# Kernel optimization log

Measured on AMD Instinct MI355X. Metric: run time of the kernel, lower is better.

## Reference

```python
import jax, jax.numpy as jnp
import numpy as np

N = 100000
E = 1600000
IN_F = 16
OUT_F = 16
HEADS = 6
ALPHA_COEFF = 0.2
NEG_SLOPE = 0.2


def setup_inputs() -> dict:
    key = jax.random.key(0)
    k1, k2, k3, k4, k5, k6 = jax.random.split(key, 6)
    data = jax.random.uniform(k1, (N, IN_F), dtype=jnp.float32)
    edge_index = jax.random.randint(k2, (2, E), 0, N, dtype=jnp.int64)
    # GATConv params (glorot-ish scale)
    W = jax.random.normal(k3, (IN_F, HEADS * OUT_F), dtype=jnp.float32) * (1.0 / np.sqrt(IN_F))
    att_src = jax.random.normal(k4, (1, HEADS, OUT_F), dtype=jnp.float32) * (1.0 / np.sqrt(OUT_F))
    att_dst = jax.random.normal(k5, (1, HEADS, OUT_F), dtype=jnp.float32) * (1.0 / np.sqrt(OUT_F))
    bias = jnp.zeros((OUT_F,), dtype=jnp.float32)
    return {"data": data, "edge_index": edge_index, "W": W,
            "att_src": att_src, "att_dst": att_dst, "bias": bias}


def _gat_deformer(data, edge_index, W, att_src, att_dst, bias):
    n = data.shape[0]
    # add self loops (PyG GATConv default add_self_loops=True)
    loop = jnp.arange(n, dtype=edge_index.dtype)
    src = jnp.concatenate([edge_index[0], loop])  # [E']
    dst = jnp.concatenate([edge_index[1], loop])  # [E']

    x = (data @ W).reshape(n, HEADS, OUT_F)          # [N,H,C]
    a_src = jnp.sum(x * att_src, axis=-1)            # [N,H]
    a_dst = jnp.sum(x * att_dst, axis=-1)            # [N,H]

    e = a_src[src] + a_dst[dst]                      # [E',H]
    e = jnp.where(e > 0, e, NEG_SLOPE * e)           # leaky_relu(0.2)
    # segment softmax over destination nodes (PyG softmax, +1e-16 denom)
    seg_max = jax.ops.segment_max(e, dst, num_segments=n)
    e = jnp.exp(e - seg_max[dst])
    seg_sum = jax.ops.segment_sum(e, dst, num_segments=n)
    alpha = e / (seg_sum[dst] + 1e-16)               # [E',H]

    # first pass: weighted scatter-add of transformed features
    out = jax.ops.segment_sum(x[src] * alpha[:, :, None], dst, num_segments=n)  # [N,H,C]
    feat = out.mean(axis=1) + bias                   # concat=False -> head mean, + bias

    # second propagate: reuse (scaled) attention on raw coordinates
    coord = data[:, :2]                              # [N,2]
    alpha2 = alpha * ALPHA_COEFF                     # [E',H]
    msg = coord[src][:, None, :] * alpha2[:, :, None]  # [E',H,2]
    out_coord = jax.ops.segment_sum(msg, dst, num_segments=n).mean(axis=1)  # [N,2]

    # fix boundary nodes (masks computed from input coords)
    up = data[:, 0] == 1.0
    down = data[:, 0] == 0.0
    left = data[:, 1] == 0.0
    right = data[:, 1] == 1.0
    c0 = jnp.where(up, 1.0, jnp.where(down, 0.0, out_coord[:, 0]))
    c1 = jnp.where(right, 1.0, jnp.where(left, 0.0, out_coord[:, 1]))
    out_coord = jnp.stack([c0, c1], axis=1)

    feat = jax.nn.selu(feat)
    return out_coord, feat


def reference(data, edge_index, W, att_src, att_dst, bias):
    return _gat_deformer(data, edge_index, W, att_src, att_dst, bias)
```

## Files before the change

kernel.cpp:

```cpp
#include <hip/hip_runtime.h>
#include <hip/hip_fp16.h>
#include <math.h>

#define N_NODES 100000
#define N_EDGES 1600000
#define E_TOT (N_EDGES + N_NODES)
#define IN_FEAT 16
#define OUT_FEAT 16
#define HEADS 6
#define HF 96

#define NB 4096
#define NBA 4000
#define NPB 25
#define CAP 576
#define MAXDEG 64
#define NBLK_PART 256
#define NT_BLOCKS ((N_NODES * HEADS + 255) / 256)

static __device__ __forceinline__ unsigned int pk2h(float a, float b) {
    return (unsigned int)__half_as_ushort(__float2half_rn(a))
         | ((unsigned int)__half_as_ushort(__float2half_rn(b)) << 16);
}

__global__ void prep(const int* __restrict__ esrc,
                     const int* __restrict__ edst,
                     int* __restrict__ gcursor,
                     unsigned int* __restrict__ spack,
                     const float* __restrict__ data,
                     const float* __restrict__ W,
                     const float* __restrict__ att_src,
                     const float* __restrict__ att_dst,
                     float* __restrict__ a_srcF,
                     float* __restrict__ a_dstF,
                     unsigned short* __restrict__ data_f16) {
    __shared__ int shmem[2 * NB];

    if (blockIdx.x < NBLK_PART) {
        int* hist = shmem;
        int* base = shmem + NB;
        const int chunk = (E_TOT + NBLK_PART - 1) / NBLK_PART;
        const int e0 = blockIdx.x * chunk;
        const int e1 = min(e0 + chunk, E_TOT);

        for (int j = threadIdx.x; j < NB; j += blockDim.x) hist[j] = 0;
        __syncthreads();
        for (int e = e0 + threadIdx.x; e < e1; e += blockDim.x) {
            int d = (e < N_EDGES) ? edst[e] : (e - N_EDGES);
            atomicAdd(&hist[d / NPB], 1);
        }
        __syncthreads();
        for (int j = threadIdx.x; j < NB; j += blockDim.x) {
            int c = hist[j];
            base[j] = c ? atomicAdd(&gcursor[j], c) : 0;
        }
        __syncthreads();
        for (int j = threadIdx.x; j < NB; j += blockDim.x) hist[j] = 0;
        __syncthreads();
        for (int e = e0 + threadIdx.x; e < e1; e += blockDim.x) {
            int s, d;
            if (e < N_EDGES) { s = esrc[e]; d = edst[e]; }
            else             { s = d = e - N_EDGES; }
            int b = d / NPB;
            int r = atomicAdd(&hist[b], 1);
            int pos = b * CAP + base[b] + r;
            if (pos < (b + 1) * CAP)
                spack[pos] = (unsigned int)s | ((unsigned int)(d - b * NPB) << 17);
        }
    } else {
        float* sW  = (float*)shmem;
        float* sAs = sW + IN_FEAT * HF;
        float* sAd = sAs + HF;
        for (int i = threadIdx.x; i < IN_FEAT * HF; i += blockDim.x) sW[i] = W[i];
        for (int i = threadIdx.x; i < HF; i += blockDim.x) { sAs[i] = att_src[i]; sAd[i] = att_dst[i]; }
        __syncthreads();

        int gid = (blockIdx.x - NBLK_PART) * blockDim.x + threadIdx.x;
        int n = gid / HEADS;
        int h = gid % HEADS;
        if (n >= N_NODES) return;

        float dv[IN_FEAT];
        const float4* dp = (const float4*)(data + (size_t)n * IN_FEAT);
#pragma unroll
        for (int q = 0; q < 4; q++) {
            float4 v = dp[q];
            dv[q*4+0] = v.x; dv[q*4+1] = v.y; dv[q*4+2] = v.z; dv[q*4+3] = v.w;
        }

        if (h < 4) {
            uint2 pkd;
            pkd.x = pk2h(dv[h*4+0], dv[h*4+1]);
            pkd.y = pk2h(dv[h*4+2], dv[h*4+3]);
            *(uint2*)(data_f16 + (size_t)n * IN_FEAT + h * 4) = pkd;
        }

        float outv[OUT_FEAT];
#pragma unroll
        for (int fo = 0; fo < OUT_FEAT; fo++) outv[fo] = 0.f;
#pragma unroll
        for (int k = 0; k < IN_FEAT; k++) {
            float dk = dv[k];
            const float* wrow = &sW[k * HF + h * OUT_FEAT];
#pragma unroll
            for (int fo = 0; fo < OUT_FEAT; fo++) outv[fo] = fmaf(dk, wrow[fo], outv[fo]);
        }

        float as = 0.f, ad = 0.f;
#pragma unroll
        for (int fo = 0; fo < OUT_FEAT; fo++) {
            as = fmaf(outv[fo], sAs[h * OUT_FEAT + fo], as);
            ad = fmaf(outv[fo], sAd[h * OUT_FEAT + fo], ad);
        }
        a_srcF[n * 8 + h] = as;
        a_dstF[n * 8 + h] = ad;
        if (h == 0) {
            a_srcF[n * 8 + 6] = 0.f; a_srcF[n * 8 + 7] = 0.f;
            a_dstF[n * 8 + 6] = 0.f; a_dstF[n * 8 + 7] = 0.f;
        }
    }
}

__global__ __launch_bounds__(256, 4)
void bucket_accumulate(const int* __restrict__ gcursor,
                       const unsigned int* __restrict__ spack,
                       const float* __restrict__ data,
                       const unsigned short* __restrict__ data_f16,
                       const float* __restrict__ a_srcF,
                       const float* __restrict__ a_dstF,
                       const float* __restrict__ W,
                       const float* __restrict__ bias,
                       float* __restrict__ out) {
    const int b = blockIdx.x;
    const int n0 = b * NPB;
    __shared__ unsigned int olist[NPB * MAXDEG];
    __shared__ float wsn_l[NPB * 100];
    __shared__ int cnt[NPB];
    __shared__ int nidx;

    const int tid  = threadIdx.x;
    const int lane = tid & 63;
    const int slot = lane >> 4;
    const int f    = lane & 15;
    const int sbase = lane & 48;

    int ecnt = gcursor[b];
    if (ecnt > CAP) ecnt = CAP;

    for (int j = tid; j < NPB; j += 256) cnt[j] = 0;
    if (tid == 0) nidx = 0;
    __syncthreads();

    for (int i = tid; i < ecnt; i += 256) {
        unsigned int p = spack[b * CAP + i];
        int dl = (int)(p >> 17);
        int r = atomicAdd(&cnt[dl], 1);
        if (r < MAXDEG)
            olist[dl * MAXDEG + r] = p & 0x1FFFFu;
    }
    __syncthreads();

    for (;;) {
        int my;
        if (lane == 0) my = atomicAdd(&nidx, 1);
        my = __builtin_amdgcn_readfirstlane(my);
        if (my >= NPB) break;

        int T = cnt[my];
        if (T > MAXDEG) T = MAXDEG;
        const unsigned int* ol = olist + my * MAXDEG;

        float adh = 0.f;
        if (f < HEADS) adh = a_dstF[(n0 + my) * 8 + f];

        float ws[HEADS], dn[HEADS];
#pragma unroll
        for (int h = 0; h < HEADS; h++) { ws[h] = 0.f; dn[h] = 0.f; }

        for (int t = slot; t < T; t += 4) {
            int s = (int)ol[t];
            float dv = __half2float(__ushort_as_half(data_f16[(size_t)s * IN_FEAT + f]));
            float exv = 0.f;
            if (f < HEADS) {
                float e = a_srcF[s * 8 + f] + adh;
                e = fmaxf(e, 0.2f * e);
                exv = __expf(e);
            }
            float e0 = __shfl(exv, sbase + 0);
            float e1 = __shfl(exv, sbase + 1);
            float e2 = __shfl(exv, sbase + 2);
            float e3 = __shfl(exv, sbase + 3);
            float e4 = __shfl(exv, sbase + 4);
            float e5 = __shfl(exv, sbase + 5);
            ws[0] = fmaf(dv, e0, ws[0]); dn[0] += e0;
            ws[1] = fmaf(dv, e1, ws[1]); dn[1] += e1;
            ws[2] = fmaf(dv, e2, ws[2]); dn[2] += e2;
            ws[3] = fmaf(dv, e3, ws[3]); dn[3] += e3;
            ws[4] = fmaf(dv, e4, ws[4]); dn[4] += e4;
            ws[5] = fmaf(dv, e5, ws[5]); dn[5] += e5;
        }

#pragma unroll
        for (int h = 0; h < HEADS; h++) {
            ws[h] += __shfl_xor(ws[h], 16);
            ws[h] += __shfl_xor(ws[h], 32);
            dn[h] += __shfl_xor(dn[h], 16);
            dn[h] += __shfl_xor(dn[h], 32);
        }

        if (slot == 0) {
            const int n = n0 + my;
            float cs = 0.f;
#pragma unroll
            for (int h = 0; h < HEADS; h++) {
                float wsn = ws[h] * __builtin_amdgcn_rcpf(dn[h] + 1e-16f);
                cs += wsn;
                wsn_l[my * 100 + h * 16 + f] = wsn;
            }
            if (f < 2) {
                float c = cs * (0.2f / 6.f);
                float key = data[(size_t)n * IN_FEAT + f];
                if (key == 1.0f)      c = 1.0f;
                else if (key == 0.0f) c = 0.0f;
                out[n * 2 + f] = c;
            }
        }
    }
    __syncthreads();

    const float sc = 1.0507009873554805f;
    const float al = 1.6732632423543772f;
    for (int task = tid; task < NPB * 16; task += 256) {
        int dl = task >> 4, fo = task & 15;
        float acc = 0.f;
#pragma unroll
        for (int h = 0; h < HEADS; h++) {
            const float* wr = wsn_l + dl * 100 + h * 16;
            const float* Wc = W + h * 16 + fo;
#pragma unroll
            for (int k = 0; k < IN_FEAT; k++)
                acc = fmaf(wr[k], Wc[k * HF], acc);
        }
        float v = acc * (1.f / 6.f) + bias[fo];
        v = v > 0.f ? sc * v : sc * al * (__expf(v) - 1.f);
        out[2 * N_NODES + (size_t)(n0 + dl) * OUT_FEAT + fo] = v;
    }
}

extern "C" void kernel_launch(void* const* d_in, const int* in_sizes, int n_in,
                              void* d_out, int out_size, void* d_ws, size_t ws_size,
                              hipStream_t stream) {
    const float* data    = (const float*)d_in[0];
    const int*   eidx    = (const int*)d_in[1];
    const float* W       = (const float*)d_in[2];
    const float* att_src = (const float*)d_in[3];
    const float* att_dst = (const float*)d_in[4];
    const float* bias    = (const float*)d_in[5];
    float*       out     = (float*)d_out;
    float*       ws      = (float*)d_ws;

    float*          a_srcF   = ws;
    float*          a_dstF   = ws + 800008;
    int*            gcursor  = (int*)(ws + 1600016);
    unsigned int*   spack    = (unsigned int*)(ws + 1604112);
    unsigned short* data_f16 = (unsigned short*)(ws + 3963408);

    hipMemsetAsync(gcursor, 0, NB * sizeof(int), stream);

    prep<<<NBLK_PART + NT_BLOCKS, 256, 0, stream>>>(
        eidx, eidx + N_EDGES, gcursor, spack,
        data, W, att_src, att_dst, a_srcF, a_dstF, data_f16);

    bucket_accumulate<<<NBA, 256, 0, stream>>>(
        gcursor, spack, data, data_f16, a_srcF, a_dstF, W, bias, out);
}
```

Baseline: 155.1 us.

## Fuse per-node feature projection into the wave loop using a transposed weight table

Moves the final feat = wsn·W projection out of a block-wide post-pass and into each wave's per-node loop. A per-wave shared buffer replaces the per-block wsn array, and the 96x16 dot product is split across the four 16-lane slots and reduced with shuffles. A transposed copy of W (MT) is written once by prep so the inner loop reads contiguous rows. It also drops the launch_bounds(256,4) hint and removes the extra block-wide barrier and the larger shared array. The trade-off is that each wave now does the projection serially per node and reads MT from global memory or cache repeatedly.

Result: slower. 160.1 us (+3.2%).

```diff
diff --git a/kernel.cpp b/kernel.cpp
--- a/kernel.cpp
+++ b/kernel.cpp
@@ -33,7 +33,8 @@
                      const float* __restrict__ att_dst,
                      float* __restrict__ a_srcF,
                      float* __restrict__ a_dstF,
-                     unsigned short* __restrict__ data_f16) {
+                     unsigned short* __restrict__ data_f16,
+                     float* __restrict__ MT) {
     __shared__ int shmem[2 * NB];
 
     if (blockIdx.x < NBLK_PART) {
@@ -75,6 +76,13 @@
         for (int i = threadIdx.x; i < HF; i += blockDim.x) { sAs[i] = att_src[i]; sAd[i] = att_dst[i]; }
         __syncthreads();
 
+        if (blockIdx.x == NBLK_PART) {
+            for (int idx = threadIdx.x; idx < HF * 16; idx += blockDim.x) {
+                int j = idx >> 4, fo = idx & 15;
+                MT[idx] = sW[(j & 15) * HF + (j >> 4) * 16 + fo];
+            }
+        }
+
         int gid = (blockIdx.x - NBLK_PART) * blockDim.x + threadIdx.x;
         int n = gid / HEADS;
         int h = gid % HEADS;
@@ -121,20 +129,19 @@
     }
 }
 
-__global__ __launch_bounds__(256, 4)
-void bucket_accumulate(const int* __restrict__ gcursor,
-                       const unsigned int* __restrict__ spack,
-                       const float* __restrict__ data,
-                       const unsigned short* __restrict__ data_f16,
-                       const float* __restrict__ a_srcF,
-                       const float* __restrict__ a_dstF,
-                       const float* __restrict__ W,
-                       const float* __restrict__ bias,
-                       float* __restrict__ out) {
+__global__ void bucket_accumulate(const int* __restrict__ gcursor,
+                                  const unsigned int* __restrict__ spack,
+                                  const float* __restrict__ data,
+                                  const unsigned short* __restrict__ data_f16,
+                                  const float* __restrict__ a_srcF,
+                                  const float* __restrict__ a_dstF,
+                                  const float* __restrict__ MT,
+                                  const float* __restrict__ bias,
+                                  float* __restrict__ out) {
     const int b = blockIdx.x;
     const int n0 = b * NPB;
     __shared__ unsigned int olist[NPB * MAXDEG];
-    __shared__ float wsn_l[NPB * 100];
+    __shared__ float wsn_w[4][104];
     __shared__ int cnt[NPB];
     __shared__ int nidx;
 
@@ -143,6 +150,7 @@
     const int slot = lane >> 4;
     const int f    = lane & 15;
     const int sbase = lane & 48;
+    const int wv   = tid >> 6;
 
     int ecnt = gcursor[b];
     if (ecnt > CAP) ecnt = CAP;
@@ -160,18 +168,21 @@
     }
     __syncthreads();
 
+    const float sc = 1.0507009873554805f;
+    const float al = 1.6732632423543772f;
     for (;;) {
         int my;
         if (lane == 0) my = atomicAdd(&nidx, 1);
         my = __builtin_amdgcn_readfirstlane(my);
         if (my >= NPB) break;
+        const int n = n0 + my;
 
         int T = cnt[my];
         if (T > MAXDEG) T = MAXDEG;
         const unsigned int* ol = olist + my * MAXDEG;
 
         float adh = 0.f;
-        if (f < HEADS) adh = a_dstF[(n0 + my) * 8 + f];
+        if (f < HEADS) adh = a_dstF[(size_t)n * 8 + f];
 
         float ws[HEADS], dn[HEADS];
 #pragma unroll
@@ -182,7 +193,7 @@
             float dv = __half2float(__ushort_as_half(data_f16[(size_t)s * IN_FEAT + f]));
             float exv = 0.f;
             if (f < HEADS) {
-                float e = a_srcF[s * 8 + f] + adh;
+                float e = a_srcF[(size_t)s * 8 + f] + adh;
                 e = fmaxf(e, 0.2f * e);
                 exv = __expf(e);
             }
@@ -209,13 +220,12 @@
         }
 
         if (slot == 0) {
-            const int n = n0 + my;
             float cs = 0.f;
 #pragma unroll
             for (int h = 0; h < HEADS; h++) {
                 float wsn = ws[h] * __builtin_amdgcn_rcpf(dn[h] + 1e-16f);
                 cs += wsn;
-                wsn_l[my * 100 + h * 16 + f] = wsn;
+                wsn_w[wv][h * 16 + f] = wsn;
             }
             if (f < 2) {
                 float c = cs * (0.2f / 6.f);
@@ -225,25 +235,22 @@
                 out[n * 2 + f] = c;
             }
         }
-    }
-    __syncthreads();
-
-    const float sc = 1.0507009873554805f;
-    const float al = 1.6732632423543772f;
-    for (int task = tid; task < NPB * 16; task += 256) {
-        int dl = task >> 4, fo = task & 15;
+
+        const float* wr = wsn_w[wv];
+        const int jbase = slot * 24;
         float acc = 0.f;
 #pragma unroll
-        for (int h = 0; h < HEADS; h++) {
-            const float* wr = wsn_l + dl * 100 + h * 16;
-            const float* Wc = W + h * 16 + fo;
-#pragma unroll
-            for (int k = 0; k < IN_FEAT; k++)
-                acc = fmaf(wr[k], Wc[k * HF], acc);
-        }
-        float v = acc * (1.f / 6.f) + bias[fo];
-        v = v > 0.f ? sc * v : sc * al * (__expf(v) - 1.f);
-        out[2 * N_NODES + (size_t)(n0 + dl) * OUT_FEAT + fo] = v;
+        for (int jj = 0; jj < 24; jj++) {
+            int j = jbase + jj;
+            acc = fmaf(wr[j], MT[j * 16 + f], acc);
+        }
+        acc += __shfl_xor(acc, 16);
+        acc += __shfl_xor(acc, 32);
+        if (slot == 0) {
+            float v = acc * (1.f / 6.f) + bias[f];
+            v = v > 0.f ? sc * v : sc * al * (__expf(v) - 1.f);
+            out[2 * N_NODES + (size_t)n * OUT_FEAT + f] = v;
+        }
     }
 }
 
@@ -264,13 +271,14 @@
     int*            gcursor  = (int*)(ws + 1600016);
     unsigned int*   spack    = (unsigned int*)(ws + 1604112);
     unsigned short* data_f16 = (unsigned short*)(ws + 3963408);
+    float*          MT       = ws + 4763408;
 
     hipMemsetAsync(gcursor, 0, NB * sizeof(int), stream);
 
     prep<<<NBLK_PART + NT_BLOCKS, 256, 0, stream>>>(
         eidx, eidx + N_EDGES, gcursor, spack,
-        data, W, att_src, att_dst, a_srcF, a_dstF, data_f16);
+        data, W, att_src, att_dst, a_srcF, a_dstF, data_f16, MT);
 
     bucket_accumulate<<<NBA, 256, 0, stream>>>(
-        gcursor, spack, data, data_f16, a_srcF, a_dstF, W, bias, out);
-}
+        gcursor, spack, data, data_f16, a_srcF, a_dstF, MT, bias, out);
+}
```
